# Kernel optimization log

Hardware: AMD Instinct MI355X
Metric: run time of the kernel (lower is better)

The kernel has to match this reference:

```python
import jax, jax.numpy as jnp
import numpy as np

N_HEADS = 32
N_KV = 8
HEAD_DIM = 128
EPS = 1e-5

def _rope(t, fr, fi):
    # t: [b,s,h,hd] -> pairs [b,s,h,hd/2,2]; fr/fi: [s,hd/2]
    tp = t.astype(jnp.float32).reshape(*t.shape[:-1], HEAD_DIM // 2, 2)
    a, b = tp[..., 0], tp[..., 1]
    fr = fr[None, :, None, :]
    fi = fi[None, :, None, :]
    out = jnp.stack([a * fr - b * fi, a * fi + b * fr], axis=-1)
    return out.reshape(t.shape).astype(t.dtype)

def _rmsnorm(t):
    tf = t.astype(jnp.float32)
    return (tf * jax.lax.rsqrt(jnp.mean(tf * tf, axis=-1, keepdims=True) + EPS)).astype(t.dtype)

def setup_inputs() -> dict:
    key = jax.random.key(0)
    ks = jax.random.split(key, 5)
    b, s, dim = 1, 2048, 4096
    x = jax.random.normal(ks[0], (b, s, dim), dtype=jnp.float32) * 0.02
    wq = jax.random.normal(ks[1], (dim, dim), dtype=jnp.float32) * 0.02
    wk = jax.random.normal(ks[2], (N_KV * HEAD_DIM, dim), dtype=jnp.float32) * 0.02
    wv = jax.random.normal(ks[3], (N_KV * HEAD_DIM, dim), dtype=jnp.float32) * 0.02
    wo = jax.random.normal(ks[4], (dim, dim), dtype=jnp.float32) * 0.02
    # RoPE freqs, llama-style theta=10000
    inv = 1.0 / (10000.0 ** (np.arange(0, HEAD_DIM, 2, dtype=np.float32) / HEAD_DIM))
    ang = np.outer(np.arange(s, dtype=np.float32), inv)  # [s, hd/2]
    freqs_cis = jnp.asarray(np.stack([np.cos(ang), np.sin(ang)], axis=-1))  # [s, hd/2, 2]
    # causal additive mask
    mask = jnp.where(jnp.tril(jnp.ones((s, s), dtype=bool)), 0.0, -1e30).astype(jnp.float32)
    return {"x": x, "wq": wq, "wk": wk, "wv": wv, "wo": wo,
            "freqs_cis": freqs_cis, "mask": mask, "start_pos": 0}

def reference(x, wq, wk, wv, wo, freqs_cis, mask, start_pos):
    b, s, dim = x.shape
    n_rep = N_HEADS // N_KV
    xq = jnp.einsum('bsd,ed->bse', x, wq).reshape(b, s, N_HEADS, HEAD_DIM)
    xk = jnp.einsum('bsd,ed->bse', x, wk).reshape(b, s, N_KV, HEAD_DIM)
    xv = jnp.einsum('bsd,ed->bse', x, wv).reshape(b, s, N_KV, HEAD_DIM)
    fr, fi = freqs_cis[..., 0], freqs_cis[..., 1]
    xq = _rope(xq, fr, fi)
    xk = _rope(xk, fr, fi)
    xq = _rmsnorm(xq)
    xk = _rmsnorm(xk)
    # start_pos=0 prefill: KV cache write/read is identity on xk/xv
    q = xq.transpose(0, 2, 1, 3).reshape(b, N_KV, n_rep, s, HEAD_DIM)  # grouped query heads
    k = xk.transpose(0, 2, 1, 3)  # [b, n_kv, s, hd]
    v = xv.transpose(0, 2, 1, 3)
    scores = jnp.einsum('bkrsd,bktd->bkrst', q, k) / np.sqrt(HEAD_DIM)
    scores = scores + mask[None, None, None, :, :]
    probs = jax.nn.softmax(scores, axis=-1)
    o = jnp.einsum('bkrst,bktd->bkrsd', probs, v)
    o = o.reshape(b, N_HEADS, s, HEAD_DIM).transpose(0, 2, 1, 3).reshape(b, s, dim)
    return jnp.einsum('bse,de->bsd', o, wo)
```

## Files before the change

### kernel.cpp

```cpp
#include <hip/hip_runtime.h>
#include <hip/hip_bf16.h>
#include <cstdint>
#include <cstddef>

using u16 = unsigned short;
using u32 = unsigned int;

typedef __attribute__((ext_vector_type(8))) __bf16 bf16x8;
typedef __attribute__((ext_vector_type(4))) float f32x4;
typedef __attribute__((ext_vector_type(2))) float f32x2;
typedef __attribute__((ext_vector_type(4))) u32 u32x4;

typedef const __attribute__((address_space(1))) void* gas_ptr;
typedef __attribute__((address_space(3))) void* las_ptr;

__device__ __forceinline__ void async_cp16(const void* g, void* l) {
  __builtin_amdgcn_global_load_lds((gas_ptr)g, (las_ptr)l, 16, 0, 0);
}

__device__ __forceinline__ float bf2f(u16 u) {
  u32 v = ((u32)u) << 16;
  return __builtin_bit_cast(float, v);
}
__device__ __forceinline__ u16 f2bf(float f) {
  u32 v = __builtin_bit_cast(u32, f);
  u32 r = (v + 0x7fffu + ((v >> 16) & 1u)) >> 16;
  return (u16)r;
}

__device__ __forceinline__ f32x4 mfma16(bf16x8 a, bf16x8 b, f32x4 c) {
  return __builtin_amdgcn_mfma_f32_16x16x32_bf16(a, b, c, 0, 0, 0);
}

__global__ __launch_bounds__(256) void cvt_f32_bf16(const float* __restrict__ in,
                                                    u16* __restrict__ out, int n8) {
  int i = blockIdx.x * blockDim.x + threadIdx.x;
  int stride = gridDim.x * blockDim.x;
  for (; i < n8; i += stride) {
    const float4* p = (const float4*)(in + (size_t)i * 8);
    float4 a = p[0], b = p[1];
    union { u16 us[8]; u32x4 v; } o;
    o.us[0] = f2bf(a.x); o.us[1] = f2bf(a.y); o.us[2] = f2bf(a.z); o.us[3] = f2bf(a.w);
    o.us[4] = f2bf(b.x); o.us[5] = f2bf(b.y); o.us[6] = f2bf(b.z); o.us[7] = f2bf(b.w);
    *(u32x4*)(out + (size_t)i * 8) = o.v;
  }
}

template <bool F32OUT>
__global__ __launch_bounds__(256) void gemm_bt(const u16* __restrict__ A,
                                               const u16* __restrict__ B,
                                               void* __restrict__ Cv,
                                               int M, int N, int K) {
  __shared__ __align__(16) u16 As[128 * 32];
  __shared__ __align__(16) u16 Bs[128 * 32];
  const int tid = threadIdx.x;
  const int wave = tid >> 6, lane = tid & 63;
  const int quad = lane >> 4, c16 = lane & 15;
  const int m0 = blockIdx.y * 128, n0 = blockIdx.x * 128;
  const int wm = (wave & 1) * 64, wn = (wave >> 1) * 64;

  f32x4 acc[4][4] = {};

  const int arow = tid >> 2;
  const int aseg = (tid & 3) ^ ((tid >> 3) & 3);
  const u16* Ab = A + (size_t)m0 * K;
  const u16* Bb = B + (size_t)n0 * K;

  for (int k0 = 0; k0 < K; k0 += 32) {
    __syncthreads();
    async_cp16(Ab + (size_t)arow * K + k0 + aseg * 8, As + (size_t)tid * 8);
    async_cp16(Ab + (size_t)(arow + 64) * K + k0 + aseg * 8, As + (size_t)(tid + 256) * 8);
    async_cp16(Bb + (size_t)arow * K + k0 + aseg * 8, Bs + (size_t)tid * 8);
    async_cp16(Bb + (size_t)(arow + 64) * K + k0 + aseg * 8, Bs + (size_t)(tid + 256) * 8);
    asm volatile("s_waitcnt vmcnt(0)" ::: "memory");
    __syncthreads();

    bf16x8 af[4], bfr[4];
#pragma unroll
    for (int mt = 0; mt < 4; ++mt) {
      int row = wm + mt * 16 + c16;
      int slot = row * 4 + (quad ^ ((row >> 1) & 3));
      af[mt] = *(const bf16x8*)(As + slot * 8);
    }
#pragma unroll
    for (int nt = 0; nt < 4; ++nt) {
      int row = wn + nt * 16 + c16;
      int slot = row * 4 + (quad ^ ((row >> 1) & 3));
      bfr[nt] = *(const bf16x8*)(Bs + slot * 8);
    }
#pragma unroll
    for (int mt = 0; mt < 4; ++mt)
#pragma unroll
      for (int nt = 0; nt < 4; ++nt)
        acc[mt][nt] = mfma16(af[mt], bfr[nt], acc[mt][nt]);
  }

#pragma unroll
  for (int mt = 0; mt < 4; ++mt) {
#pragma unroll
    for (int nt = 0; nt < 4; ++nt) {
#pragma unroll
      for (int r = 0; r < 4; ++r) {
        int gm = m0 + wm + mt * 16 + quad * 4 + r;
        int gn = n0 + wn + nt * 16 + c16;
        float v = acc[mt][nt][r];
        if (F32OUT)
          ((float*)Cv)[(size_t)gm * N + gn] = v;
        else
          ((u16*)Cv)[(size_t)gm * N + gn] = f2bf(v);
      }
    }
  }
}

__global__ __launch_bounds__(256) void transpose_v(const u16* __restrict__ in,
                                                   u16* __restrict__ out) {
  __shared__ __align__(16) u16 t[64 * 72];
  const int bs = blockIdx.x * 64;
  const int be = blockIdx.y * 64;
  const int tid = threadIdx.x;
  {
    const int row = tid >> 3, cc = tid & 7;
#pragma unroll
    for (int pp = 0; pp < 2; ++pp) {
      int r = row + 32 * pp;
      u32x4 v = *(const u32x4*)(in + (size_t)(bs + r) * 6144 + 5120 + be + cc * 8);
      *(u32x4*)(&t[r * 72 + ((cc ^ ((r >> 3) & 7)) * 8)]) = v;
    }
  }
  __syncthreads();
  {
    const int c0 = tid >> 3, rc = tid & 7;
#pragma unroll
    for (int pp = 0; pp < 2; ++pp) {
      int c = c0 + 32 * pp;
      union { u16 us[8]; u32x4 v; } o;
#pragma unroll
      for (int j = 0; j < 8; ++j)
        o.us[j] = t[(rc * 8 + j) * 72 + ((((c >> 3) ^ rc) * 8) + (c & 7))];
      *(u32x4*)(out + (size_t)(be + c) * 2048 + bs + rc * 8) = o.v;
    }
  }
}

__global__ __launch_bounds__(256) void rope_rms(const u16* __restrict__ in, int stride,
                                                u16* __restrict__ out,
                                                const float* __restrict__ freqs,
                                                int n_heads) {
  int gw = blockIdx.x * 4 + (threadIdx.x >> 6);
  int lane = threadIdx.x & 63;
  int s = gw / n_heads, h = gw % n_heads;
  u32 ab = *(const u32*)(in + (size_t)s * stride + h * 128 + lane * 2);
  float a = bf2f((u16)(ab & 0xffff));
  float b = bf2f((u16)(ab >> 16));
  f32x2 ff = *(const f32x2*)(freqs + (size_t)s * 128 + lane * 2);
  float ra = a * ff.x - b * ff.y;
  float rb = a * ff.y + b * ff.x;
  float ss = ra * ra + rb * rb;
#pragma unroll
  for (int m = 32; m; m >>= 1) ss += __shfl_xor(ss, m, 64);
  float r = rsqrtf(ss * (1.0f / 128.0f) + 1e-5f);
  u32 pk = (u32)f2bf(ra * r) | ((u32)f2bf(rb * r) << 16);
  *(u32*)(out + ((size_t)h * 2048 + s) * 128 + lane * 2) = pk;
}

#define SEQ 2048
__global__ __launch_bounds__(256) void attn(const u16* __restrict__ Q,
                                            const u16* __restrict__ Kh,
                                            const u16* __restrict__ VT,
                                            u16* __restrict__ O) {
  __shared__ __align__(16) u16 Ks[2][64 * 128];
  __shared__ __align__(16) u16 Vs[2][128 * 64];
  __shared__ __align__(16) u16 Ps[4][32 * 64];
  const int tid = threadIdx.x;
  const int wave = tid >> 6, lane = tid & 63;
  const int quad = lane >> 4, c16 = lane & 15;
  const int bid = blockIdx.x;
  const int hk = bid & 7;
  const int rest = bid >> 3;
  const int hq = rest >> 3;
  const int p = rest & 7;
  const int h = hk * 4 + hq;

  const float sc = 0.12751743f;
  const float B = 16.5f;
  const u16* Kb = Kh + (size_t)hk * SEQ * 128;
  const u16* Vb = VT + (size_t)hk * 128 * SEQ;

  auto stage = [&](int t0, int b) __attribute__((always_inline)) {
#pragma unroll
    for (int i = 0; i < 4; ++i) {
      int idx = tid + 256 * i;
      int row = idx >> 4, sg = (idx & 15) ^ (row & 7);
      async_cp16(Kb + (size_t)(t0 + row) * 128 + sg * 8, &Ks[b][(size_t)idx * 8]);
    }
#pragma unroll
    for (int i = 0; i < 4; ++i) {
      int idx = tid + 256 * i;
      int row = idx >> 3, sg = (idx & 7) ^ (row & 7);
      async_cp16(Vb + (size_t)row * SEQ + t0 + sg * 8, &Vs[b][(size_t)idx * 8]);
    }
  };

#pragma unroll 1
  for (int tile = 0; tile < 2; ++tile) {
    const int qt = tile ? (15 - p) : p;
    const int q0w = qt * 128 + wave * 32;
    const int kend = qt * 128 + 128;

    bf16x8 qfr[2][4];
    const u16* qbase = Q + (size_t)h * SEQ * 128;
#pragma unroll
    for (int g = 0; g < 2; ++g)
#pragma unroll
      for (int c = 0; c < 4; ++c)
        qfr[g][c] =
            *(const bf16x8*)(qbase + (size_t)(q0w + g * 16 + c16) * 128 + c * 32 + quad * 8);

    f32x4 o_acc[2][8] = {};
    float lsum[2][4] = {};

    __syncthreads();
    stage(0, 0);

#pragma unroll 1
    for (int t0 = 0; t0 < kend; t0 += 64) {
      const int cur = (t0 >> 6) & 1;
      asm volatile("s_waitcnt vmcnt(0)" ::: "memory");
      __syncthreads();
      if (t0 + 64 < kend) stage(t0 + 64, cur ^ 1);

      if (t0 < q0w + 32) {
        f32x4 sa[2][4] = {};
#pragma unroll
        for (int ct = 0; ct < 4; ++ct) {
          int t = ct * 16 + c16;
          int tbase = t * 128;
          int tsw = t & 7;
#pragma unroll
          for (int c = 0; c < 4; ++c) {
            bf16x8 kf = *(const bf16x8*)(&Ks[cur][tbase + (((c * 4 + quad) ^ tsw) * 8)]);
            sa[0][ct] = mfma16(qfr[0][c], kf, sa[0][ct]);
            sa[1][ct] = mfma16(qfr[1][c], kf, sa[1][ct]);
          }
        }

        const bool diag = (t0 + 64 > q0w);
        auto soft = [&](bool masked) __attribute__((always_inline)) {
#pragma unroll
          for (int g = 0; g < 2; ++g) {
#pragma unroll
            for (int r = 0; r < 4; ++r) {
              int row = g * 16 + quad * 4 + r;
              int row_q = q0w + row;
              int rbase = row * 64;
              int rsw = row & 7;
#pragma unroll
              for (int ct = 0; ct < 4; ++ct) {
                float s = sa[g][ct][r];
                float arg = fmaf(s, sc, -B);
                if (masked) {
                  int t_idx = t0 + ct * 16 + c16;
                  arg = (t_idx <= row_q) ? arg : -1.0e30f;
                }
                float pe = exp2f(arg);
                lsum[g][r] += pe;
                u32 pb = (__builtin_bit_cast(u32, pe) + 0x8000u) >> 16;
                Ps[wave][rbase + (((ct * 2 + (c16 >> 3)) ^ rsw) * 8) + (c16 & 7)] = (u16)pb;
              }
            }
          }
        };
        if (diag) soft(true); else soft(false);
        asm volatile("s_waitcnt lgkmcnt(0)" ::: "memory");

#pragma unroll
        for (int tc = 0; tc < 2; ++tc) {
          bf16x8 pf[2];
#pragma unroll
          for (int g = 0; g < 2; ++g) {
            int prow = g * 16 + c16;
            pf[g] = *(const bf16x8*)(&Ps[wave][prow * 64 + (((tc * 4 + quad) ^ (prow & 7)) * 8)]);
          }
#pragma unroll
          for (int nt = 0; nt < 8; ++nt) {
            int dl = nt * 16 + c16;
            bf16x8 vf = *(const bf16x8*)(&Vs[cur][dl * 64 + (((tc * 4 + quad) ^ (dl & 7)) * 8)]);
            o_acc[0][nt] = mfma16(pf[0], vf, o_acc[0][nt]);
            o_acc[1][nt] = mfma16(pf[1], vf, o_acc[1][nt]);
          }
        }
      }
    }

#pragma unroll
    for (int g = 0; g < 2; ++g) {
#pragma unroll
      for (int r = 0; r < 4; ++r) {
        float l = lsum[g][r];
#pragma unroll
        for (int m = 1; m < 16; m <<= 1) l += __shfl_xor(l, m, 64);
        float inv = 1.0f / l;
        int s_idx = q0w + g * 16 + quad * 4 + r;
        u16* ob = O + (size_t)s_idx * 4096 + (size_t)h * 128;
#pragma unroll
        for (int nt = 0; nt < 8; ++nt) ob[nt * 16 + c16] = f2bf(o_acc[g][nt][r] * inv);
      }
    }
  }
}

extern "C" void kernel_launch(void* const* d_in, const int* in_sizes, int n_in,
                              void* d_out, int out_size, void* d_ws, size_t ws_size,
                              hipStream_t stream) {
  const float* x  = (const float*)d_in[0];
  const float* wq = (const float*)d_in[1];
  const float* wk = (const float*)d_in[2];
  const float* wv = (const float*)d_in[3];
  const float* wo = (const float*)d_in[4];
  const float* fr = (const float*)d_in[5];
  float* out = (float*)d_out;

  const size_t S = 2048, D = 4096, KV = 1024, NQKV = D + 2 * KV;
  u16* p = (u16*)d_ws;
  u16* xb     = p; p += S * D;
  u16* wqkv   = p; p += NQKV * D;
  u16* qkvraw = p; p += S * NQKV;
  u16* qh     = p; p += S * D;
  u16* khh    = p; p += S * KV;
  u16* vt     = p; p += KV * S;
  u16* wob = wqkv;
  u16* ob  = qkvraw;

  auto cvt_launch = [&](const float* src, u16* dst, size_t n) {
    int n8 = (int)(n / 8);
    int blocks = (n8 + 255) / 256;
    if (blocks > 2048) blocks = 2048;
    cvt_f32_bf16<<<dim3(blocks), dim3(256), 0, stream>>>(src, dst, n8);
  };

  cvt_launch(x, xb, S * D);
  cvt_launch(wq, wqkv, D * D);
  cvt_launch(wk, wqkv + D * D, KV * D);
  cvt_launch(wv, wqkv + (D + KV) * D, KV * D);

  gemm_bt<false><<<dim3(NQKV / 128, S / 128), dim3(256), 0, stream>>>(
      xb, wqkv, (void*)qkvraw, (int)S, (int)NQKV, (int)D);

  cvt_launch(wo, wob, D * D);

  transpose_v<<<dim3(32, 16), dim3(256), 0, stream>>>(qkvraw, vt);
  rope_rms<<<dim3((int)(S * 32 / 4)), dim3(256), 0, stream>>>(qkvraw, (int)NQKV, qh, fr, 32);
  rope_rms<<<dim3((int)(S * 8 / 4)), dim3(256), 0, stream>>>(qkvraw + D, (int)NQKV, khh, fr, 8);

  attn<<<dim3(256), dim3(256), 0, stream>>>(qh, khh, vt, ob);

  gemm_bt<true><<<dim3(D / 128, S / 128), dim3(256), 0, stream>>>(ob, wob, (void*)out,
                                                                  (int)S, (int)D, (int)D);
}
```

Before: 546.1 us.

## Deepen GEMM K-tile to 64 and remap blocks for XCD-local L2 reuse

The GEMM K-step grows from 32 to 64, so each shared-memory load and barrier round feeds twice as many MFMAs, and the LDS swizzle is changed to an 8-way XOR. The grid is flattened to 1D and block indices are remapped so each of the 8 XCDs handles a contiguous range of N tiles and sweeps over M, which keeps weight tiles local to one L2. Launch bounds now request 3 blocks per CU. The cost is 32KB of LDS per block and more fragment registers, which could limit occupancy. The remap also assumes N/128 divides evenly by 8.

```diff
diff --git a/kernel.cpp b/kernel.cpp
--- a/kernel.cpp
+++ b/kernel.cpp
@@ -47,52 +47,68 @@
 }
 
 template <bool F32OUT>
-__global__ __launch_bounds__(256) void gemm_bt(const u16* __restrict__ A,
-                                               const u16* __restrict__ B,
-                                               void* __restrict__ Cv,
-                                               int M, int N, int K) {
-  __shared__ __align__(16) u16 As[128 * 32];
-  __shared__ __align__(16) u16 Bs[128 * 32];
+__global__ __launch_bounds__(256, 3) void gemm_bt(const u16* __restrict__ A,
+                                                  const u16* __restrict__ B,
+                                                  void* __restrict__ Cv,
+                                                  int M, int N, int K) {
+  __shared__ __align__(16) u16 As[128 * 64];
+  __shared__ __align__(16) u16 Bs[128 * 64];
   const int tid = threadIdx.x;
   const int wave = tid >> 6, lane = tid & 63;
   const int quad = lane >> 4, c16 = lane & 15;
-  const int m0 = blockIdx.y * 128, n0 = blockIdx.x * 128;
+
+  const int mb = M >> 7, nb = N >> 7;
+  const int per_xcd_n = nb >> 3;
+  const int xcd = blockIdx.x & 7, lid = blockIdx.x >> 3;
+  const int m_t = lid % mb, n_local = lid / mb;
+  const int m0 = m_t * 128, n0 = (xcd * per_xcd_n + n_local) * 128;
+
   const int wm = (wave & 1) * 64, wn = (wave >> 1) * 64;
 
   f32x4 acc[4][4] = {};
 
-  const int arow = tid >> 2;
-  const int aseg = (tid & 3) ^ ((tid >> 3) & 3);
   const u16* Ab = A + (size_t)m0 * K;
   const u16* Bb = B + (size_t)n0 * K;
 
-  for (int k0 = 0; k0 < K; k0 += 32) {
+  for (int k0 = 0; k0 < K; k0 += 64) {
     __syncthreads();
-    async_cp16(Ab + (size_t)arow * K + k0 + aseg * 8, As + (size_t)tid * 8);
-    async_cp16(Ab + (size_t)(arow + 64) * K + k0 + aseg * 8, As + (size_t)(tid + 256) * 8);
-    async_cp16(Bb + (size_t)arow * K + k0 + aseg * 8, Bs + (size_t)tid * 8);
-    async_cp16(Bb + (size_t)(arow + 64) * K + k0 + aseg * 8, Bs + (size_t)(tid + 256) * 8);
+#pragma unroll
+    for (int i = 0; i < 4; ++i) {
+      int idx = tid + 256 * i;
+      int row = idx >> 3, sg = (idx & 7) ^ (row & 7);
+      async_cp16(Ab + (size_t)row * K + k0 + sg * 8, As + (size_t)idx * 8);
+    }
+#pragma unroll
+    for (int i = 0; i < 4; ++i) {
+      int idx = tid + 256 * i;
+      int row = idx >> 3, sg = (idx & 7) ^ (row & 7);
+      async_cp16(Bb + (size_t)row * K + k0 + sg * 8, Bs + (size_t)idx * 8);
+    }
     asm volatile("s_waitcnt vmcnt(0)" ::: "memory");
     __syncthreads();
 
-    bf16x8 af[4], bfr[4];
+    bf16x8 af[4][2], bfr[4][2];
 #pragma unroll
     for (int mt = 0; mt < 4; ++mt) {
       int row = wm + mt * 16 + c16;
-      int slot = row * 4 + (quad ^ ((row >> 1) & 3));
-      af[mt] = *(const bf16x8*)(As + slot * 8);
+#pragma unroll
+      for (int c = 0; c < 2; ++c)
+        af[mt][c] = *(const bf16x8*)(As + row * 64 + (((c * 4 + quad) ^ (row & 7)) * 8));
     }
 #pragma unroll
     for (int nt = 0; nt < 4; ++nt) {
       int row = wn + nt * 16 + c16;
-      int slot = row * 4 + (quad ^ ((row >> 1) & 3));
-      bfr[nt] = *(const bf16x8*)(Bs + slot * 8);
-    }
-#pragma unroll
-    for (int mt = 0; mt < 4; ++mt)
-#pragma unroll
-      for (int nt = 0; nt < 4; ++nt)
-        acc[mt][nt] = mfma16(af[mt], bfr[nt], acc[mt][nt]);
+#pragma unroll
+      for (int c = 0; c < 2; ++c)
+        bfr[nt][c] = *(const bf16x8*)(Bs + row * 64 + (((c * 4 + quad) ^ (row & 7)) * 8));
+    }
+#pragma unroll
+    for (int c = 0; c < 2; ++c)
+#pragma unroll
+      for (int mt = 0; mt < 4; ++mt)
+#pragma unroll
+        for (int nt = 0; nt < 4; ++nt)
+          acc[mt][nt] = mfma16(af[mt][c], bfr[nt][c], acc[mt][nt]);
   }
 
 #pragma unroll
@@ -344,7 +360,7 @@
   cvt_launch(wk, wqkv + D * D, KV * D);
   cvt_launch(wv, wqkv + (D + KV) * D, KV * D);
 
-  gemm_bt<false><<<dim3(NQKV / 128, S / 128), dim3(256), 0, stream>>>(
+  gemm_bt<false><<<dim3((S / 128) * (NQKV / 128)), dim3(256), 0, stream>>>(
       xb, wqkv, (void*)qkvraw, (int)S, (int)NQKV, (int)D);
 
   cvt_launch(wo, wob, D * D);
@@ -355,6 +371,6 @@
 
   attn<<<dim3(256), dim3(256), 0, stream>>>(qh, khh, vt, ob);
 
-  gemm_bt<true><<<dim3(D / 128, S / 128), dim3(256), 0, stream>>>(ob, wob, (void*)out,
-                                                                  (int)S, (int)D, (int)D);
-}
+  gemm_bt<true><<<dim3((S / 128) * (D / 128)), dim3(256), 0, stream>>>(
+      ob, wob, (void*)out, (int)S, (int)D, (int)D);
+}
```

After: 484.7 us. -11.2%, faster.
